# Kernel optimization log

Measured on AMD Instinct MI355X. Metric: run time of the kernel, lower is better.

Reference implementation:

```python
import jax, jax.numpy as jnp
import numpy as np

N, IN_DIM, HID, HEADS, OUT_DIM = 4096, 512, 128, 4, 64
ALPHA = 0.2
NEG_INF = -9e15  # matches torch's -9000000000000000.0 fill


def _gat_layer(adj_mask, h, W, a, concat):
    # h: [N, Fin], W: [Fin, Fout], a: [2*Fout, 1]
    Wh = h @ W                                   # [N, Fout]
    f_out = W.shape[1]
    Wh1 = Wh @ a[:f_out]                         # [N, 1]
    Wh2 = Wh @ a[f_out:]                         # [N, 1]
    e = jax.nn.leaky_relu(Wh1 + Wh2.T, ALPHA)    # [N, N] broadcast scores
    e = jnp.where(adj_mask, e, NEG_INF)
    att = jax.nn.softmax(e, axis=1)              # masked row softmax
    out = att @ Wh                               # [N, Fout] aggregate
    return jax.nn.elu(out) if concat else out


def setup_inputs() -> dict:
    key = jax.random.key(0)
    k = jax.random.split(key, 6)
    g = jax.random.randint(k[0], (N, N), 0, 2, dtype=jnp.int32)
    inputs = jax.random.normal(k[1], (N, IN_DIM), dtype=jnp.float32)
    # xavier-uniform-like scales
    s1 = np.sqrt(6.0 / (IN_DIM + HID)) * 1.414
    sa1 = np.sqrt(6.0 / (2 * HID + 1)) * 1.414
    s2 = np.sqrt(6.0 / (HID * HEADS + OUT_DIM)) * 1.414
    sa2 = np.sqrt(6.0 / (2 * OUT_DIM + 1)) * 1.414
    W1 = jax.random.uniform(k[2], (HEADS, IN_DIM, HID), jnp.float32, -s1, s1)
    a1 = jax.random.uniform(k[3], (HEADS, 2 * HID, 1), jnp.float32, -sa1, sa1)
    W2 = jax.random.uniform(k[4], (HID * HEADS, OUT_DIM), jnp.float32, -s2, s2)
    a2 = jax.random.uniform(k[5], (2 * OUT_DIM, 1), jnp.float32, -sa2, sa2)
    return {"g": g, "inputs": inputs, "W1": W1, "a1": a1, "W2": W2, "a2": a2}


def reference(g, inputs, W1, a1, W2, a2):
    adj_mask = g > 0                                              # [N, N] bool
    # layer 1: HEADS parallel heads, concat=True (elu), then concat on features
    heads_out = jax.vmap(lambda W, a: _gat_layer(adj_mask, inputs, W, a, True))(W1, a1)
    h = jnp.transpose(heads_out, (1, 0, 2)).reshape(N, HEADS * HID)  # [N, H*HID]
    # output attention layer, concat=False (no elu)
    return _gat_layer(adj_mask, h, W2, a2, False)                 # [N, OUT_DIM]
```

## Files before the change

kernel.cpp:

```cpp
#include <hip/hip_runtime.h>
#include <hip/hip_bf16.h>
#include <stdint.h>

#define NN 4096
#define KD 512
#define LOG2E 1.4426950408889634f

typedef __attribute__((ext_vector_type(8))) short short8;
typedef __attribute__((ext_vector_type(4))) float f32x4;

__device__ __forceinline__ float lrelu(float x) { return fmaxf(x, 0.2f * x); }

__device__ __forceinline__ unsigned short f2bf(float f) {
    uint32_t u = __float_as_uint(f);
    u += 0x7fff + ((u >> 16) & 1);
    return (unsigned short)(u >> 16);
}

__device__ __forceinline__ float exp2_fast(float x) {
    float r; asm("v_exp_f32 %0, %1" : "=v"(r) : "v"(x)); return r;
}

__device__ __forceinline__ uint32_t cvt_pk_bf16(float lo, float hi) {
    uint32_t r; asm("v_cvt_pk_bf16_f32 %0, %1, %2" : "=v"(r) : "v"(lo), "v"(hi)); return r;
}

__device__ __forceinline__ void glds16(const void* g, void* l) {
    __builtin_amdgcn_global_load_lds(
        (const __attribute__((address_space(1))) uint32_t*)g,
        (__attribute__((address_space(3))) uint32_t*)l, 16, 0, 0);
}

__global__ void k_bitmask(const int* __restrict__ g, uint64_t* __restrict__ bm) {
    int wave = threadIdx.x >> 6;
    int lane = threadIdx.x & 63;
    int row = blockIdx.x * 4 + wave;
    const int* grow = g + (size_t)row * NN;
    for (int w = 0; w < 64; ++w) {
        int v = grow[w * 64 + lane];
        unsigned long long m = __ballot(v > 0);
        if (lane == 0) bm[(size_t)row * 64 + w] = m;
    }
}

__global__ void k_cast(const float* __restrict__ x, unsigned short* __restrict__ y, int n4) {
    int i = blockIdx.x * 256 + threadIdx.x;
    if (i < n4) {
        float4 v = ((const float4*)x)[i];
        uint2 o;
        o.x = (uint32_t)f2bf(v.x) | ((uint32_t)f2bf(v.y) << 16);
        o.y = (uint32_t)f2bf(v.z) | ((uint32_t)f2bf(v.w) << 16);
        ((uint2*)y)[i] = o;
    }
}

__global__ __launch_bounds__(256)
void k_tc(const float* __restrict__ src, unsigned short* __restrict__ dst, int R, int C) {
    __shared__ float tile[64][65];
    int b = blockIdx.z;
    int r0 = blockIdx.x * 64, c0 = blockIdx.y * 64;
    src += (size_t)b * R * C;
    dst += (size_t)b * C * R;
    int t = threadIdx.x;
    #pragma unroll
    for (int s = 0; s < 16; ++s) {
        int idx = t + s * 256;
        int r = idx >> 6, c = idx & 63;
        tile[r][c] = src[(size_t)(r0 + r) * C + c0 + c];
    }
    __syncthreads();
    #pragma unroll
    for (int s = 0; s < 16; ++s) {
        int idx = t + s * 256;
        int r = idx >> 6, c = idx & 63;
        dst[(size_t)(c0 + r) * R + r0 + c] = f2bf(tile[c][r]);
    }
}

template <int F>
__global__ __launch_bounds__(512)
void k_gemm_fused(const unsigned short* __restrict__ Abf, const unsigned short* __restrict__ WT,
                  const float* __restrict__ avec,
                  unsigned short* __restrict__ WhT, float* __restrict__ s1g,
                  float* __restrict__ s2g, unsigned int* __restrict__ smaxKey) {
    constexpr int BM = 32, BK = 64;
    constexpr int NCF = F / 64;
    __shared__ unsigned short a_lds[2][BM * BK];
    __shared__ unsigned short b_lds[2][F * BK];
    __shared__ unsigned short t_lds[F * 40];
    __shared__ float sred[BM][2];
    int t = threadIdx.x, lane = t & 63, w = t >> 6;
    int h = blockIdx.y;
    int i0 = blockIdx.x * BM;
    const unsigned short* WTh = WT + (size_t)h * F * KD;
    int r0 = (w >> 2) * 16, c0 = (w & 3) * (F / 4);
    int krow = lane & 15, kgrp = lane >> 4;
    if (t < BM) { sred[t][0] = 0.f; sred[t][1] = 0.f; }
    f32x4 acc[NCF];
    #pragma unroll
    for (int cf = 0; cf < NCF; ++cf) acc[cf] = (f32x4){0.f, 0.f, 0.f, 0.f};

    auto stage = [&](int buf, int kt) {
        int k0 = kt * BK;
        if (w < 4) {
            int c = w * 64 + lane;
            int row = c >> 3, slot = c & 7;
            glds16(Abf + (size_t)(i0 + row) * KD + k0 + ((slot ^ (row & 7)) * 8),
                   &a_lds[buf][(w * 64) * 8]);
        }
        #pragma unroll
        for (int s = 0; s < F / 64; ++s) {
            int c = w * F + s * 64 + lane;
            int row = c >> 3, slot = c & 7;
            glds16(WTh + (size_t)row * KD + k0 + ((slot ^ (row & 7)) * 8),
                   &b_lds[buf][(w * F + s * 64) * 8]);
        }
    };

    stage(0, 0);
    __syncthreads();
    int cur = 0;
    for (int kt = 0; kt < KD / BK; ++kt) {
        int nxt = cur ^ 1;
        if (kt + 1 < KD / BK) stage(nxt, kt + 1);
        #pragma unroll
        for (int ks = 0; ks < 2; ++ks) {
            int koff = ks * 32 + kgrp * 8;
            int arow = r0 + krow;
            short8 av = *(const short8*)((const char*)&a_lds[cur][arow * BK] +
                                         ((koff * 2) ^ ((arow & 7) << 4)));
            #pragma unroll
            for (int cf = 0; cf < NCF; ++cf) {
                int brow = c0 + cf * 16 + krow;
                short8 bv = *(const short8*)((const char*)&b_lds[cur][brow * BK] +
                                             ((koff * 2) ^ ((brow & 7) << 4)));
                acc[cf] = __builtin_amdgcn_mfma_f32_16x16x32_bf16(av, bv, acc[cf], 0, 0, 0);
            }
        }
        __syncthreads();
        cur = nxt;
    }
    float p1[4] = {0.f, 0.f, 0.f, 0.f}, p2[4] = {0.f, 0.f, 0.f, 0.f};
    const float* ah = avec + (size_t)h * 2 * F;
    #pragma unroll
    for (int cf = 0; cf < NCF; ++cf) {
        int col = c0 + cf * 16 + krow;
        float aw1 = ah[col], aw2 = ah[F + col];
        #pragma unroll
        for (int r = 0; r < 4; ++r) {
            int row = r0 + kgrp * 4 + r;
            t_lds[col * 40 + row] = f2bf(acc[cf][r]);
            p1[r] += acc[cf][r] * aw1;
            p2[r] += acc[cf][r] * aw2;
        }
    }
    #pragma unroll
    for (int d = 1; d < 16; d <<= 1) {
        #pragma unroll
        for (int r = 0; r < 4; ++r) { p1[r] += __shfl_xor(p1[r], d); p2[r] += __shfl_xor(p2[r], d); }
    }
    if (krow == 0) {
        #pragma unroll
        for (int r = 0; r < 4; ++r) {
            int row = r0 + kgrp * 4 + r;
            atomicAdd(&sred[row][0], p1[r]);
            atomicAdd(&sred[row][1], p2[r]);
        }
    }
    __syncthreads();
    {
        int col = t >> 2, seg = (t & 3) * 8;
        if (col < F) {
            uint4 v = *(const uint4*)&t_lds[col * 40 + seg];
            *(uint4*)&WhT[((size_t)h * F + col) * NN + i0 + seg] = v;
        }
    }
    if (t < BM) {
        s1g[(size_t)h * NN + i0 + t] = sred[t][0] * LOG2E;
        s2g[(size_t)h * NN + i0 + t] = sred[t][1] * LOG2E;
    }
    if (w == 0) {
        float v = (t < BM) ? sred[t][1] * LOG2E : -3.4e38f;
        #pragma unroll
        for (int d = 1; d < 64; d <<= 1) v = fmaxf(v, __shfl_xor(v, d));
        if (lane == 0) {
            uint32_t b = __float_as_uint(v);
            uint32_t key = (b & 0x80000000u) ? ~b : (b | 0x80000000u);
            atomicMax(smaxKey + h, key);
        }
    }
}

template <int F, int NW, int NJH>
__global__ __launch_bounds__(NW * 64, 4)
void k_agg3(const unsigned short* __restrict__ WhT, const float* __restrict__ s1v,
            const float* __restrict__ s2v, const unsigned int* __restrict__ smaxKey,
            const unsigned char* __restrict__ bmb,
            float* __restrict__ pnum, float* __restrict__ pden, int njt, int nh) {
    constexpr int TI = (NW / NJH) * 32, TJ = NJH * 32;
    constexpr int NB = F / 16;
    constexpr int CPR = TJ / 8;
    constexpr int CH_W = F * CPR / NW;
    constexpr int XF = F + 4;
    constexpr int XROWS = TI / 2;
    constexpr size_t ST_BYTES = sizeof(unsigned short) * 3 * F * TJ;
    constexpr size_t XCH_BYTES = sizeof(float) * (size_t)(NJH - 1) * XROWS * XF;
    constexpr size_t SM_BYTES = ST_BYTES > XCH_BYTES ? ST_BYTES : XCH_BYTES;
    __shared__ __align__(16) char smem[SM_BYTES];
    __shared__ float den_sh[NJH][TI];
    auto whT_lds = (unsigned short (*)[F * TJ])smem;
    float* xch = (float*)smem;
    int t = threadIdx.x, l = t & 63, w = t >> 6;
    int h = blockIdx.y, js = blockIdx.z;
    int i0 = blockIdx.x * TI;
    int rg = w / NJH, jh = w % NJH;
    int r0 = rg * 32;
    const unsigned short* WhTh = WhT + (size_t)h * F * NN;
    const float* s2h = s2v + (size_t)h * NN;
    unsigned int kk = smaxKey[h];
    float smax = __uint_as_float((kk & 0x80000000u) ? (kk ^ 0x80000000u) : ~kk);
    int rowA = i0 + r0 + (l & 15);
    int rowB = rowA + 16;
    float s1A = s1v[(size_t)h * NN + rowA];
    float s1B = s1v[(size_t)h * NN + rowB];
    float miA = lrelu(s1A + smax), miB = lrelu(s1B + smax);
    float c1A = s1A - miA, c2A = fmaf(0.2f, s1A, -miA);
    float c1B = s1B - miB, c2B = fmaf(0.2f, s1B, -miB);
    int joff = jh * 32 + (l >> 4) * 8;
    int jsbase = js * njt;
    const unsigned char* bmbA = bmb + (size_t)rowA * 512;
    const unsigned char* bmbB = bmb + (size_t)rowB * 512;

    f32x4 acc[2][NB];
    #pragma unroll
    for (int m = 0; m < 2; ++m)
        #pragma unroll
        for (int b = 0; b < NB; ++b) acc[m][b] = (f32x4){0.f, 0.f, 0.f, 0.f};
    float denA = 0.f, denB = 0.f;

    struct SD { float4 q0, q1; unsigned int mA, mB; };
    struct PA { short8 a, b; };

    auto loadSD = [&](int jt) {
        SD s;
        int j0 = (jsbase + jt) * TJ;
        s.q0 = *(const float4*)&s2h[j0 + joff];
        s.q1 = *(const float4*)&s2h[j0 + joff + 4];
        int wb = (jsbase + jt) * CPR + jh * 4 + (l >> 4);
        s.mA = bmbA[wb];
        s.mB = bmbB[wb];
        return s;
    };

    auto computeP = [&](const SD& s) {
        float q[8] = {s.q0.x, s.q0.y, s.q0.z, s.q0.w, s.q1.x, s.q1.y, s.q1.z, s.q1.w};
        float pA[8], pB[8];
        #pragma unroll
        for (int u = 0; u < 8; ++u) {
            float tA = fmaxf(q[u] + c1A, fmaf(0.2f, q[u], c2A));
            float vA = ((s.mA >> u) & 1u) ? exp2_fast(tA) : 0.f;
            denA += vA; pA[u] = vA;
            float tB = fmaxf(q[u] + c1B, fmaf(0.2f, q[u], c2B));
            float vB = ((s.mB >> u) & 1u) ? exp2_fast(tB) : 0.f;
            denB += vB; pB[u] = vB;
        }
        union { uint32_t d[4]; short8 v; } ua, ub;
        #pragma unroll
        for (int j = 0; j < 4; ++j) {
            ua.d[j] = cvt_pk_bf16(pA[2 * j], pA[2 * j + 1]);
            ub.d[j] = cvt_pk_bf16(pB[2 * j], pB[2 * j + 1]);
        }
        PA p; p.a = ua.v; p.b = ub.v;
        return p;
    };

    auto stage = [&](int buf, int jt) {
        int j0 = (jsbase + jt) * TJ;
        #pragma unroll
        for (int s = 0; s < CH_W / 64; ++s) {
            int c = w * CH_W + s * 64 + l;
            int row = c / CPR, slot = c % CPR;
            glds16(WhTh + (size_t)row * NN + j0 + ((slot ^ (row & 7)) * 8),
                   &whT_lds[buf][(w * CH_W + s * 64) * 8]);
        }
    };

    auto domfma = [&](int buf, const PA& pa) {
        #pragma unroll
        for (int b = 0; b < NB; ++b) {
            int brow = b * 16 + (l & 15);
            short8 bv = *(const short8*)((const char*)&whT_lds[buf][brow * TJ] +
                         ((jh * 64 + (l >> 4) * 16) ^ ((brow & 7) << 4)));
            acc[0][b] = __builtin_amdgcn_mfma_f32_16x16x32_bf16(pa.a, bv, acc[0][b], 0, 0, 0);
            acc[1][b] = __builtin_amdgcn_mfma_f32_16x16x32_bf16(pa.b, bv, acc[1][b], 0, 0, 0);
        }
    };

    SD sd_cur = loadSD(0);
    stage(0, 0);
    SD sd_nxt;
    if (njt > 1) sd_nxt = loadSD(1);
    PA pa_cur = computeP(sd_cur);
    __syncthreads();
    int cur = 0, nx1 = 1;
    for (int jt = 0; jt < njt; ++jt) {
        bool more = jt + 1 < njt;
        if (more) stage(nx1, jt + 1);
        SD sd2;
        if (jt + 2 < njt) sd2 = loadSD(jt + 2);
        PA pa_n;
        if (more) pa_n = computeP(sd_nxt);
        __syncthreads();
        domfma(cur, pa_cur);
        pa_cur = pa_n;
        sd_nxt = sd2;
        cur = nx1;
        nx1 = nx1 + 1 == 3 ? 0 : nx1 + 1;
    }

    denA += __shfl_xor(denA, 16); denA += __shfl_xor(denA, 32);
    denB += __shfl_xor(denB, 16); denB += __shfl_xor(denB, 32);
    if (l < 16) {
        den_sh[jh][r0 + l] = denA;
        den_sh[jh][r0 + 16 + l] = denB;
    }
    __syncthreads();

    float* pnumS = pnum + ((size_t)(js * nh + h) * NN + i0) * F;
    #pragma unroll
    for (int m = 0; m < 2; ++m) {
        if (jh > 0) {
            float* sl = xch + (size_t)(jh - 1) * XROWS * XF;
            #pragma unroll
            for (int b = 0; b < NB; ++b) {
                int col = b * 16 + (l & 15);
                #pragma unroll
                for (int r = 0; r < 4; ++r)
                    sl[(rg * 16 + (l >> 4) * 4 + r) * XF + col] = acc[m][b][r];
            }
        }
        __syncthreads();
        if (jh == 0) {
            #pragma unroll
            for (int b = 0; b < NB; ++b) {
                int col = b * 16 + (l & 15);
                #pragma unroll
                for (int r = 0; r < 4; ++r) {
                    int lrow = rg * 16 + (l >> 4) * 4 + r;
                    int row = r0 + m * 16 + (l >> 4) * 4 + r;
                    float v = acc[m][b][r];
                    #pragma unroll
                    for (int sX = 1; sX < NJH; ++sX)
                        v += xch[((size_t)(sX - 1) * XROWS + lrow) * XF + col];
                    pnumS[(size_t)row * F + col] = v;
                }
            }
        }
        __syncthreads();
    }
    if (t < TI) {
        float d = den_sh[0][t];
        #pragma unroll
        for (int sX = 1; sX < NJH; ++sX) d += den_sh[sX][t];
        pden[(size_t)(js * nh + h) * NN + i0 + t] = d;
    }
}

__global__ void k_reduce1(const float* __restrict__ pnum, const float* __restrict__ pden,
                          unsigned short* __restrict__ hbuf) {
    int idx = blockIdx.x * 256 + threadIdx.x;
    int i = idx >> 7;
    int c4 = idx & 127;
    int hh = c4 >> 5, f4 = c4 & 31;
    float4 a = *(const float4*)&pnum[((size_t)hh * NN + i) * 128 + f4 * 4];
    float4 b = *(const float4*)&pnum[((size_t)(4 + hh) * NN + i) * 128 + f4 * 4];
    float den = pden[(size_t)hh * NN + i] + pden[(size_t)(4 + hh) * NN + i];
    float inv = 1.f / den;
    float v[4] = {(a.x + b.x) * inv, (a.y + b.y) * inv, (a.z + b.z) * inv, (a.w + b.w) * inv};
    uint2 o;
    unsigned short e[4];
    #pragma unroll
    for (int u = 0; u < 4; ++u) {
        float x = v[u];
        x = x > 0.f ? x : expm1f(x);
        e[u] = f2bf(x);
    }
    o.x = (uint32_t)e[0] | ((uint32_t)e[1] << 16);
    o.y = (uint32_t)e[2] | ((uint32_t)e[3] << 16);
    *(uint2*)&hbuf[(size_t)i * 512 + c4 * 4] = o;
}

__global__ void k_reduce2(const float* __restrict__ pnum, const float* __restrict__ pden,
                          float* __restrict__ out) {
    int idx = blockIdx.x * 256 + threadIdx.x;
    int i = idx >> 4;
    int f4 = (idx & 15) * 4;
    float4 s = {0.f, 0.f, 0.f, 0.f};
    float den = 0.f;
    #pragma unroll
    for (int js = 0; js < 8; ++js) {
        float4 v = *(const float4*)&pnum[((size_t)js * NN + i) * 64 + f4];
        s.x += v.x; s.y += v.y; s.z += v.z; s.w += v.w;
        den += pden[(size_t)js * NN + i];
    }
    float inv = 1.f / den;
    s.x *= inv; s.y *= inv; s.z *= inv; s.w *= inv;
    *(float4*)&out[(size_t)i * 64 + f4] = s;
}

extern "C" void kernel_launch(void* const* d_in, const int* in_sizes, int n_in,
                              void* d_out, int out_size, void* d_ws, size_t ws_size,
                              hipStream_t stream) {
    const int*   g      = (const int*)d_in[0];
    const float* inputs = (const float*)d_in[1];
    const float* W1     = (const float*)d_in[2];
    const float* a1     = (const float*)d_in[3];
    const float* W2     = (const float*)d_in[4];
    const float* a2     = (const float*)d_in[5];
    float* out = (float*)d_out;
    char* ws = (char*)d_ws;

    size_t off = 0;
    uint64_t* bm   = (uint64_t*)(ws + off); off += (size_t)NN * 64 * 8;
    unsigned short* Xbf  = (unsigned short*)(ws + off); off += (size_t)NN * KD * 2;
    unsigned short* W1T  = (unsigned short*)(ws + off); off += (size_t)4 * 128 * KD * 2;
    unsigned short* W2T  = (unsigned short*)(ws + off); off += (size_t)64 * KD * 2;
    unsigned short* WhT1 = (unsigned short*)(ws + off); off += (size_t)4 * 128 * NN * 2;
    unsigned short* WhT2 = (unsigned short*)(ws + off); off += (size_t)64 * NN * 2;
    unsigned short* hbuf = (unsigned short*)(ws + off); off += (size_t)NN * KD * 2;
    float* s1_1    = (float*)(ws + off);    off += (size_t)4 * NN * 4;
    float* s2_1    = (float*)(ws + off);    off += (size_t)4 * NN * 4;
    float* s1_2    = (float*)(ws + off);    off += (size_t)NN * 4;
    float* s2_2    = (float*)(ws + off);    off += (size_t)NN * 4;
    unsigned int* keys = (unsigned int*)(ws + off); off += 256;
    float* pnum    = (float*)(ws + off);    off += (size_t)8 * NN * 128 * 4;
    float* pden    = (float*)(ws + off);    off += (size_t)8 * NN * 4;
    float* pnum2 = pnum;
    float* pden2 = pden;

    hipMemsetAsync(keys, 0, 32, stream);
    k_bitmask<<<NN / 4, 256, 0, stream>>>(g, bm);
    k_cast<<<(NN * KD / 4 + 255) / 256, 256, 0, stream>>>(inputs, Xbf, NN * KD / 4);
    k_tc<<<dim3(KD / 64, 2, 4), 256, 0, stream>>>(W1, W1T, KD, 128);
    k_tc<<<dim3(KD / 64, 1, 1), 256, 0, stream>>>(W2, W2T, KD, 64);
    k_gemm_fused<128><<<dim3(NN / 32, 4), 512, 0, stream>>>(Xbf, W1T, a1, WhT1, s1_1, s2_1, keys);
    k_agg3<128, 16, 4><<<dim3(NN / 128, 4, 2), 1024, 0, stream>>>(
        WhT1, s1_1, s2_1, keys, (const unsigned char*)bm, pnum, pden, NN / 128 / 2, 4);
    k_reduce1<<<NN * 128 / 256, 256, 0, stream>>>(pnum, pden, hbuf);
    k_gemm_fused<64><<<dim3(NN / 32, 1), 512, 0, stream>>>(hbuf, W2T, a2, WhT2, s1_2, s2_2, keys + 4);
    k_agg3<64, 8, 4><<<dim3(NN / 64, 1, 8), 512, 0, stream>>>(
        WhT2, s1_2, s2_2, keys + 4, (const unsigned char*)bm, pnum2, pden2, NN / 128 / 8, 1);
    k_reduce2<<<NN * 16 / 256, 256, 0, stream>>>(pnum2, pden2, out);
}
```

Before: 124.2 us.

## Use fragment-ordered LDS layout and relax barriers to overlap staging with MFMA

The WhT tile is now staged into LDS in MFMA-fragment order (16 rows by 8-column units), replacing the XOR-swizzled row-major layout. Each 16-lane group now reads one contiguous 256-byte run, and the address math drops the swizzle. `__syncthreads` is replaced by a raw `s_barrier` with scheduling barriers, and a full `vmcnt(0)` wait is kept only on the last iteration. This aims to let the next tile's global-to-LDS prefetch stay in flight during the MFMAs, at the risk of reading LDS before the async loads land. The new global-load pattern also spreads each lane group across 16 different rows, which may coalesce worse.

```diff
diff --git a/kernel.cpp b/kernel.cpp
--- a/kernel.cpp
+++ b/kernel.cpp
@@ -199,7 +199,8 @@
             float* __restrict__ pnum, float* __restrict__ pden, int njt, int nh) {
     constexpr int TI = (NW / NJH) * 32, TJ = NJH * 32;
     constexpr int NB = F / 16;
-    constexpr int CPR = TJ / 8;
+    constexpr int TJ8 = TJ / 8;
+    constexpr int CPR = TJ8;
     constexpr int CH_W = F * CPR / NW;
     constexpr int XF = F + 4;
     constexpr int XROWS = TI / 2;
@@ -226,7 +227,8 @@
     float miA = lrelu(s1A + smax), miB = lrelu(s1B + smax);
     float c1A = s1A - miA, c2A = fmaf(0.2f, s1A, -miA);
     float c1B = s1B - miB, c2B = fmaf(0.2f, s1B, -miB);
-    int joff = jh * 32 + (l >> 4) * 8;
+    int kgrp = l >> 4;
+    int joff = jh * 32 + kgrp * 8;
     int jsbase = js * njt;
     const unsigned char* bmbA = bmb + (size_t)rowA * 512;
     const unsigned char* bmbB = bmb + (size_t)rowB * 512;
@@ -246,7 +248,7 @@
         int j0 = (jsbase + jt) * TJ;
         s.q0 = *(const float4*)&s2h[j0 + joff];
         s.q1 = *(const float4*)&s2h[j0 + joff + 4];
-        int wb = (jsbase + jt) * CPR + jh * 4 + (l >> 4);
+        int wb = (jsbase + jt) * CPR + jh * 4 + kgrp;
         s.mA = bmbA[wb];
         s.mB = bmbB[wb];
         return s;
@@ -278,9 +280,11 @@
         int j0 = (jsbase + jt) * TJ;
         #pragma unroll
         for (int s = 0; s < CH_W / 64; ++s) {
-            int c = w * CH_W + s * 64 + l;
-            int row = c / CPR, slot = c % CPR;
-            glds16(WhTh + (size_t)row * NN + j0 + ((slot ^ (row & 7)) * 8),
+            int d = w * CH_W + s * 64 + l;
+            int r = d & 15;
+            int jsl = (d >> 4) & (TJ8 - 1);
+            int b_ = d / (16 * TJ8);
+            glds16(WhTh + (size_t)(b_ * 16 + r) * NN + j0 + jsl * 8,
                    &whT_lds[buf][(w * CH_W + s * 64) * 8]);
         }
     };
@@ -288,29 +292,33 @@
     auto domfma = [&](int buf, const PA& pa) {
         #pragma unroll
         for (int b = 0; b < NB; ++b) {
-            int brow = b * 16 + (l & 15);
-            short8 bv = *(const short8*)((const char*)&whT_lds[buf][brow * TJ] +
-                         ((jh * 64 + (l >> 4) * 16) ^ ((brow & 7) << 4)));
+            int unit = (b * 16 + jh * 4 + kgrp) * 16 + (l & 15);
+            short8 bv = *(const short8*)&whT_lds[buf][unit * 8];
             acc[0][b] = __builtin_amdgcn_mfma_f32_16x16x32_bf16(pa.a, bv, acc[0][b], 0, 0, 0);
             acc[1][b] = __builtin_amdgcn_mfma_f32_16x16x32_bf16(pa.b, bv, acc[1][b], 0, 0, 0);
         }
     };
 
     SD sd_cur = loadSD(0);
+    __builtin_amdgcn_sched_barrier(0);
     stage(0, 0);
+    __builtin_amdgcn_sched_barrier(0);
     SD sd_nxt;
     if (njt > 1) sd_nxt = loadSD(1);
     PA pa_cur = computeP(sd_cur);
-    __syncthreads();
     int cur = 0, nx1 = 1;
     for (int jt = 0; jt < njt; ++jt) {
         bool more = jt + 1 < njt;
         if (more) stage(nx1, jt + 1);
+        __builtin_amdgcn_sched_barrier(0);
         SD sd2;
         if (jt + 2 < njt) sd2 = loadSD(jt + 2);
         PA pa_n;
         if (more) pa_n = computeP(sd_nxt);
-        __syncthreads();
+        __builtin_amdgcn_sched_barrier(0);
+        if (!more) asm volatile("s_waitcnt vmcnt(0)" ::: "memory");
+        __builtin_amdgcn_s_barrier();
+        __builtin_amdgcn_sched_barrier(0);
         domfma(cur, pa_cur);
         pa_cur = pa_n;
         sd_nxt = sd2;
```

After: 128.7 us. 1.04x slower.

## Replace LDS-staged aggregation with direct global B-fragment loads in smaller blocks

Applied to the files above, without the earlier changes.

The attention-aggregation kernel no longer stages WhT tiles into LDS through a triple-buffered async pipeline with block barriers. Each wave now loads its MFMA B fragments straight from global memory into registers, and blocks shrink to 256 threads covering 32 rows each, with head and j-split packed into a flattened 1D grid. This removes LDS staging, the per-iteration syncthreads and the software pipelining, relying on more resident blocks and L2 hits to hide latency. The cost is redundant global/L2 traffic, since WhT is no longer shared across row groups in LDS, and exposed load latency inside the loop.

```diff
diff --git a/kernel.cpp b/kernel.cpp
--- a/kernel.cpp
+++ b/kernel.cpp
@@ -191,45 +191,41 @@
     }
 }
 
-template <int F, int NW, int NJH>
-__global__ __launch_bounds__(NW * 64, 4)
-void k_agg3(const unsigned short* __restrict__ WhT, const float* __restrict__ s1v,
+template <int F, int NJH, int MINW>
+__global__ __launch_bounds__(256, MINW)
+void k_agg4(const unsigned short* __restrict__ WhT, const float* __restrict__ s1v,
             const float* __restrict__ s2v, const unsigned int* __restrict__ smaxKey,
             const unsigned char* __restrict__ bmb,
-            float* __restrict__ pnum, float* __restrict__ pden, int njt, int nh) {
-    constexpr int TI = (NW / NJH) * 32, TJ = NJH * 32;
+            float* __restrict__ pnum, float* __restrict__ pden,
+            int njt, int nh, int njs) {
+    constexpr int TI = 32, TJ = NJH * 32;
     constexpr int NB = F / 16;
     constexpr int CPR = TJ / 8;
-    constexpr int CH_W = F * CPR / NW;
     constexpr int XF = F + 4;
-    constexpr int XROWS = TI / 2;
-    constexpr size_t ST_BYTES = sizeof(unsigned short) * 3 * F * TJ;
-    constexpr size_t XCH_BYTES = sizeof(float) * (size_t)(NJH - 1) * XROWS * XF;
-    constexpr size_t SM_BYTES = ST_BYTES > XCH_BYTES ? ST_BYTES : XCH_BYTES;
-    __shared__ __align__(16) char smem[SM_BYTES];
+    __shared__ float xch[(NJH - 1) * 16 * XF];
     __shared__ float den_sh[NJH][TI];
-    auto whT_lds = (unsigned short (*)[F * TJ])smem;
-    float* xch = (float*)smem;
-    int t = threadIdx.x, l = t & 63, w = t >> 6;
-    int h = blockIdx.y, js = blockIdx.z;
-    int i0 = blockIdx.x * TI;
-    int rg = w / NJH, jh = w % NJH;
-    int r0 = rg * 32;
+    int t = threadIdx.x, l = t & 63, jh = t >> 6;
+    int combo = blockIdx.x & 7;
+    int h = combo / njs;
+    int js = combo % njs;
+    int i0 = (blockIdx.x >> 3) * TI;
+    int lane16 = l & 15, kgrp = l >> 4;
     const unsigned short* WhTh = WhT + (size_t)h * F * NN;
     const float* s2h = s2v + (size_t)h * NN;
     unsigned int kk = smaxKey[h];
     float smax = __uint_as_float((kk & 0x80000000u) ? (kk ^ 0x80000000u) : ~kk);
-    int rowA = i0 + r0 + (l & 15);
+    int rowA = i0 + lane16;
     int rowB = rowA + 16;
     float s1A = s1v[(size_t)h * NN + rowA];
     float s1B = s1v[(size_t)h * NN + rowB];
     float miA = lrelu(s1A + smax), miB = lrelu(s1B + smax);
     float c1A = s1A - miA, c2A = fmaf(0.2f, s1A, -miA);
     float c1B = s1B - miB, c2B = fmaf(0.2f, s1B, -miB);
-    int joff = jh * 32 + (l >> 4) * 8;
+    int joff = jh * 32 + kgrp * 8;
     int jsbase = js * njt;
     const unsigned char* bmbA = bmb + (size_t)rowA * 512;
     const unsigned char* bmbB = bmb + (size_t)rowB * 512;
+    const unsigned short* Bbase = WhTh + (size_t)lane16 * NN + joff;
 
     f32x4 acc[2][NB];
     #pragma unroll
@@ -238,30 +234,26 @@
         for (int b = 0; b < NB; ++b) acc[m][b] = (f32x4){0.f, 0.f, 0.f, 0.f};
     float denA = 0.f, denB = 0.f;
 
-    struct SD { float4 q0, q1; unsigned int mA, mB; };
-    struct PA { short8 a, b; };
-
-    auto loadSD = [&](int jt) {
-        SD s;
+    for (int jt = 0; jt < njt; ++jt) {
         int j0 = (jsbase + jt) * TJ;
-        s.q0 = *(const float4*)&s2h[j0 + joff];
-        s.q1 = *(const float4*)&s2h[j0 + joff + 4];
-        int wb = (jsbase + jt) * CPR + jh * 4 + (l >> 4);
-        s.mA = bmbA[wb];
-        s.mB = bmbB[wb];
-        return s;
-    };
-
-    auto computeP = [&](const SD& s) {
-        float q[8] = {s.q0.x, s.q0.y, s.q0.z, s.q0.w, s.q1.x, s.q1.y, s.q1.z, s.q1.w};
+        float4 q0 = *(const float4*)&s2h[j0 + joff];
+        float4 q1 = *(const float4*)&s2h[j0 + joff + 4];
+        int wb = (jsbase + jt) * CPR + jh * 4 + kgrp;
+        unsigned int mA = bmbA[wb];
+        unsigned int mB = bmbB[wb];
+        short8 bf[NB];
+        #pragma unroll
+        for (int b = 0; b < NB; ++b)
+            bf[b] = *(const short8*)(Bbase + (size_t)b * 16 * NN + j0);
+        float q[8] = {q0.x, q0.y, q0.z, q0.w, q1.x, q1.y, q1.z, q1.w};
         float pA[8], pB[8];
         #pragma unroll
         for (int u = 0; u < 8; ++u) {
             float tA = fmaxf(q[u] + c1A, fmaf(0.2f, q[u], c2A));
-            float vA = ((s.mA >> u) & 1u) ? exp2_fast(tA) : 0.f;
+            float vA = ((mA >> u) & 1u) ? exp2_fast(tA) : 0.f;
             denA += vA; pA[u] = vA;
             float tB = fmaxf(q[u] + c1B, fmaf(0.2f, q[u], c2B));
-            float vB = ((s.mB >> u) & 1u) ? exp2_fast(tB) : 0.f;
+            float vB = ((mB >> u) & 1u) ? exp2_fast(tB) : 0.f;
             denB += vB; pB[u] = vB;
         }
         union { uint32_t d[4]; short8 v; } ua, ub;
@@ -270,59 +262,18 @@
             ua.d[j] = cvt_pk_bf16(pA[2 * j], pA[2 * j + 1]);
             ub.d[j] = cvt_pk_bf16(pB[2 * j], pB[2 * j + 1]);
         }
-        PA p; p.a = ua.v; p.b = ub.v;
-        return p;
-    };
-
-    auto stage = [&](int buf, int jt) {
-        int j0 = (jsbase + jt) * TJ;
-        #pragma unroll
-        for (int s = 0; s < CH_W / 64; ++s) {
-            int c = w * CH_W + s * 64 + l;
-            int row = c / CPR, slot = c % CPR;
-            glds16(WhTh + (size_t)row * NN + j0 + ((slot ^ (row & 7)) * 8),
-                   &whT_lds[buf][(w * CH_W + s * 64) * 8]);
-        }
-    };
-
-    auto domfma = [&](int buf, const PA& pa) {
         #pragma unroll
         for (int b = 0; b < NB; ++b) {
-            int brow = b * 16 + (l & 15);
-            short8 bv = *(const short8*)((const char*)&whT_lds[buf][brow * TJ] +
-                         ((jh * 64 + (l >> 4) * 16) ^ ((brow & 7) << 4)));
-            acc[0][b] = __builtin_amdgcn_mfma_f32_16x16x32_bf16(pa.a, bv, acc[0][b], 0, 0, 0);
-            acc[1][b] = __builtin_amdgcn_mfma_f32_16x16x32_bf16(pa.b, bv, acc[1][b], 0, 0, 0);
-        }
-    };
-
-    SD sd_cur = loadSD(0);
-    stage(0, 0);
-    SD sd_nxt;
-    if (njt > 1) sd_nxt = loadSD(1);
-    PA pa_cur = computeP(sd_cur);
-    __syncthreads();
-    int cur = 0, nx1 = 1;
-    for (int jt = 0; jt < njt; ++jt) {
-        bool more = jt + 1 < njt;
-        if (more) stage(nx1, jt + 1);
-        SD sd2;
-        if (jt + 2 < njt) sd2 = loadSD(jt + 2);
-        PA pa_n;
-        if (more) pa_n = computeP(sd_nxt);
-        __syncthreads();
-        domfma(cur, pa_cur);
-        pa_cur = pa_n;
-        sd_nxt = sd2;
-        cur = nx1;
-        nx1 = nx1 + 1 == 3 ? 0 : nx1 + 1;
+            acc[0][b] = __builtin_amdgcn_mfma_f32_16x16x32_bf16(ua.v, bf[b], acc[0][b], 0, 0, 0);
+            acc[1][b] = __builtin_amdgcn_mfma_f32_16x16x32_bf16(ub.v, bf[b], acc[1][b], 0, 0, 0);
+        }
     }
 
     denA += __shfl_xor(denA, 16); denA += __shfl_xor(denA, 32);
     denB += __shfl_xor(denB, 16); denB += __shfl_xor(denB, 32);
     if (l < 16) {
-        den_sh[jh][r0 + l] = denA;
-        den_sh[jh][r0 + 16 + l] = denB;
+        den_sh[jh][l] = denA;
+        den_sh[jh][16 + l] = denB;
     }
     __syncthreads();
 
@@ -330,28 +281,28 @@
     #pragma unroll
     for (int m = 0; m < 2; ++m) {
         if (jh > 0) {
-            float* sl = xch + (size_t)(jh - 1) * XROWS * XF;
+            float* sl = xch + (size_t)(jh - 1) * 16 * XF;
             #pragma unroll
             for (int b = 0; b < NB; ++b) {
-                int col = b * 16 + (l & 15);
+                int col = b * 16 + lane16;
                 #pragma unroll
                 for (int r = 0; r < 4; ++r)
-                    sl[(rg * 16 + (l >> 4) * 4 + r) * XF + col] = acc[m][b][r];
+                    sl[(kgrp * 4 + r) * XF + col] = acc[m][b][r];
             }
         }
         __syncthreads();
         if (jh == 0) {
             #pragma unroll
             for (int b = 0; b < NB; ++b) {
-                int col = b * 16 + (l & 15);
+                int col = b * 16 + lane16;
                 #pragma unroll
                 for (int r = 0; r < 4; ++r) {
-                    int lrow = rg * 16 + (l >> 4) * 4 + r;
-                    int row = r0 + m * 16 + (l >> 4) * 4 + r;
+                    int lrow = kgrp * 4 + r;
+                    int row = m * 16 + lrow;
                     float v = acc[m][b][r];
                     #pragma unroll
                     for (int sX = 1; sX < NJH; ++sX)
-                        v += xch[((size_t)(sX - 1) * XROWS + lrow) * XF + col];
+                        v += xch[((size_t)(sX - 1) * 16 + lrow) * XF + col];
                     pnumS[(size_t)row * F + col] = v;
                 }
             }
@@ -444,11 +395,11 @@
     k_tc<<<dim3(KD / 64, 2, 4), 256, 0, stream>>>(W1, W1T, KD, 128);
     k_tc<<<dim3(KD / 64, 1, 1), 256, 0, stream>>>(W2, W2T, KD, 64);
     k_gemm_fused<128><<<dim3(NN / 32, 4), 512, 0, stream>>>(Xbf, W1T, a1, WhT1, s1_1, s2_1, keys);
-    k_agg3<128, 16, 4><<<dim3(NN / 128, 4, 2), 1024, 0, stream>>>(
-        WhT1, s1_1, s2_1, keys, (const unsigned char*)bm, pnum, pden, NN / 128 / 2, 4);
+    k_agg4<128, 4, 3><<<NN / 32 * 8, 256, 0, stream>>>(
+        WhT1, s1_1, s2_1, keys, (const unsigned char*)bm, pnum, pden, NN / 128 / 2, 4, 2);
     k_reduce1<<<NN * 128 / 256, 256, 0, stream>>>(pnum, pden, hbuf);
     k_gemm_fused<64><<<dim3(NN / 32, 1), 512, 0, stream>>>(hbuf, W2T, a2, WhT2, s1_2, s2_2, keys + 4);
-    k_agg3<64, 8, 4><<<dim3(NN / 64, 1, 8), 512, 0, stream>>>(
-        WhT2, s1_2, s2_2, keys + 4, (const unsigned char*)bm, pnum2, pden2, NN / 128 / 8, 1);
+    k_agg4<64, 4, 4><<<NN / 32 * 8, 256, 0, stream>>>(
+        WhT2, s1_2, s2_2, keys + 4, (const unsigned char*)bm, pnum2, pden2, NN / 128 / 8, 1, 8);
     k_reduce2<<<NN * 16 / 256, 256, 0, stream>>>(pnum2, pden2, out);
 }
```

After: 168.5 us. 35.7% more time.
